# Kernel optimization log

Measured on AMD Instinct MI355X. Metric: run time of the kernel, lower is better.

The kernel has to match this reference:

```python
import jax, jax.numpy as jnp
import numpy as np

B, S, H = 4, 2048, 1024
NH, HD = 16, 64
FF = 4096
EPS = 1e-5

def _ln(x, g, b):
    m = jnp.mean(x, axis=-1, keepdims=True)
    v = jnp.var(x, axis=-1, keepdims=True)
    return (x - m) * jax.lax.rsqrt(v + EPS) * g + b

def setup_inputs() -> dict:
    key = jax.random.key(0)
    ks = jax.random.split(key, 12)
    sc = 0.02
    return {
        "hidden_states": jax.random.normal(ks[0], (B, S, H), jnp.float32),
        "Wq": jax.random.normal(ks[1], (H, H), jnp.float32) * sc,
        "bq": jnp.zeros((H,), jnp.float32),
        "Wk": jax.random.normal(ks[2], (H, H), jnp.float32) * sc,
        "bk": jnp.zeros((H,), jnp.float32),
        "Wv": jax.random.normal(ks[3], (H, H), jnp.float32) * sc,
        "bv": jnp.zeros((H,), jnp.float32),
        "Wi": jax.random.normal(ks[4], (H, FF), jnp.float32) * sc,
        "bi": jnp.zeros((FF,), jnp.float32),
        "Wo": jax.random.normal(ks[5], (FF, H), jnp.float32) * sc,
        "bo": jnp.zeros((H,), jnp.float32),
        "g1": jnp.ones((H,), jnp.float32),
        "b1": jnp.zeros((H,), jnp.float32),
        "g2": jnp.ones((H,), jnp.float32),
        "b2": jnp.zeros((H,), jnp.float32),
    }

def reference(hidden_states, Wq, bq, Wk, bk, Wv, bv, Wi, bi, Wo, bo, g1, b1, g2, b2):
    x = hidden_states
    # projections -> [B, NH, S, HD]
    def split(t):
        return t.reshape(B, S, NH, HD).transpose(0, 2, 1, 3)
    q = split(x @ Wq + bq)
    k = split(x @ Wk + bk)
    v = split(x @ Wv + bv)
    scores = jnp.einsum('bhqd,bhkd->bhqk', q, k) / jnp.sqrt(jnp.float32(HD))
    probs = jax.nn.softmax(scores, axis=-1)
    ctx = jnp.einsum('bhqk,bhkd->bhqd', probs, v)
    attn_out = ctx.transpose(0, 2, 1, 3).reshape(B, S, H)
    h = _ln(x + attn_out, g1, b1)
    ffn = jax.nn.gelu(h @ Wi + bi, approximate=False) @ Wo + bo
    return _ln(h + ffn, g2, b2)
```

## Files before the change

### kernel.cpp

```cpp
#include <hip/hip_runtime.h>

#define B_  4
#define S_  2048
#define H_  1024
#define NH_ 16
#define HD_ 64
#define FF_ 4096
#define M_  (B_*S_)

typedef __bf16 bf16x8 __attribute__((ext_vector_type(8)));
typedef float  f32x4  __attribute__((ext_vector_type(4)));
typedef unsigned short ushort8v __attribute__((ext_vector_type(8)));
typedef unsigned short ushort4v __attribute__((ext_vector_type(4)));

typedef __attribute__((address_space(1))) void GVOID;
typedef __attribute__((address_space(3))) void LVOID;

__device__ __forceinline__ void g2l16(const void* g, void* l) {
  __builtin_amdgcn_global_load_lds((GVOID*)g, (LVOID*)l, 16, 0, 0);
}

#define MFMA16(a, b, c) __builtin_amdgcn_mfma_f32_16x16x32_bf16(a, b, c, 0, 0, 0)

#if __has_builtin(__builtin_amdgcn_exp2f)
#define EXP2(x) __builtin_amdgcn_exp2f(x)
#else
#define EXP2(x) exp2f(x)
#endif

__device__ __forceinline__ unsigned short f2bf(float f) {
  unsigned int u = __float_as_uint(f);
  u += 0x7fffu + ((u >> 16) & 1u);
  return (unsigned short)(u >> 16);
}
__device__ __forceinline__ float bf2f(unsigned short h) {
  return __uint_as_float(((unsigned int)h) << 16);
}

__device__ __forceinline__ float gelu_fast(float v) {
  float y = 0.7978845608f * (v + 0.044715f * v * v * v);
  float e = EXP2(y * 2.8853900818f);
  float th = 1.0f - 2.0f / (e + 1.0f);
  return 0.5f * v * (1.0f + th);
}

__device__ __forceinline__ void xcd_swz(int& bx, int& by) {
  int gx = gridDim.x;
  int flat = by * gx + bx;
  int cpx = (gx * gridDim.y) >> 3;
  int swz = (flat & 7) * cpx + (flat >> 3);
  bx = swz % gx;
  by = swz / gx;
}

__device__ __forceinline__ void xcd_swzT(int& bx, int& by) {
  int gy = gridDim.y;
  int flat = bx * gy + by;
  int cpx = (gridDim.x * gy) >> 3;
  int swz = (flat & 7) * cpx + (flat >> 3);
  by = swz % gy;
  bx = swz / gy;
}

__global__ __launch_bounds__(256) void cast_f32_bf16(const float* __restrict__ in,
                                                     unsigned short* __restrict__ out,
                                                     int n4) {
  int i = blockIdx.x * 256 + threadIdx.x;
  if (i >= n4) return;
  float4 v = reinterpret_cast<const float4*>(in)[i];
  ushort4v o;
  o[0] = f2bf(v.x); o[1] = f2bf(v.y); o[2] = f2bf(v.z); o[3] = f2bf(v.w);
  reinterpret_cast<ushort4v*>(out)[i] = o;
}

__global__ __launch_bounds__(256) void prep_weights(const float* __restrict__ Wq,
                                                    const float* __restrict__ Wk,
                                                    const float* __restrict__ Wv,
                                                    const float* __restrict__ Wi,
                                                    const float* __restrict__ Wo,
                                                    unsigned short* __restrict__ WqkvT,
                                                    unsigned short* __restrict__ WiT,
                                                    unsigned short* __restrict__ WoT) {
  __shared__ float t[32][33];
  int id = blockIdx.x;
  const float* in; unsigned short* out; int R, C, bx, by;
  if (id < 3072) {
    int seg = id >> 10, rem = id & 1023;
    in = (seg == 0) ? Wq : (seg == 1) ? Wk : Wv;
    out = WqkvT + (size_t)seg * H_ * H_;
    R = H_; C = H_;
    bx = rem & 31; by = rem >> 5;
  } else if (id < 3072 + 4096) {
    int rem = id - 3072;
    in = Wi; out = WiT; R = H_; C = FF_;
    bx = rem & 127; by = rem >> 7;
  } else {
    int rem = id - 3072 - 4096;
    in = Wo; out = WoT; R = FF_; C = H_;
    bx = rem & 31; by = rem >> 5;
  }
  bx *= 32; by *= 32;
  const int tx = threadIdx.x & 31, ty = threadIdx.x >> 5;
#pragma unroll
  for (int i = 0; i < 32; i += 8)
    t[ty + i][tx] = in[(size_t)(by + ty + i) * C + bx + tx];
  __syncthreads();
#pragma unroll
  for (int i = 0; i < 32; i += 8)
    out[(size_t)(bx + ty + i) * R + by + tx] = f2bf(t[tx][ty + i]);
}

#define ALOAD(bufv, mf, ks)                                                      \
  *reinterpret_cast<const bf16x8*>((char*)As + (bufv)*32768 + wm*16384 +         \
      ((mf)*16 + lr)*128 + (((((ks)*4 + kg)) ^ (lr & 7)) * 16))
#define BLOAD(bufv, nf, ks)                                                      \
  *reinterpret_cast<const bf16x8*>((char*)Bs + (bufv)*32768 + bh*16384 +         \
      (brow0 + (nf)*16 + lr)*128 + (((((ks)*4 + kg)) ^ (lr & 7)) * 16))

#define PH_MFMA(MF0)                                                             \
  __builtin_amdgcn_s_barrier();                                                  \
  asm volatile("s_waitcnt lgkmcnt(0)" ::: "memory");                             \
  __builtin_amdgcn_s_setprio(1);                                                 \
  _Pragma("unroll")                                                              \
  for (int nf = 0; nf < 4; ++nf) {                                               \
    acc[MF0][nf]     = MFMA16(a_[0][0], bfr[nf][0], acc[MF0][nf]);               \
    acc[MF0][nf]     = MFMA16(a_[0][1], bfr[nf][1], acc[MF0][nf]);               \
    acc[MF0 + 1][nf] = MFMA16(a_[1][0], bfr[nf][0], acc[MF0 + 1][nf]);           \
    acc[MF0 + 1][nf] = MFMA16(a_[1][1], bfr[nf][1], acc[MF0 + 1][nf]);           \
  }                                                                              \
  __builtin_amdgcn_s_setprio(0);

#define GEMM256_CORE(A_, Bt_, LDK_, NKT_, KOFF_)                                 \
  __shared__ unsigned short As[2][2][128 * 64];                                  \
  __shared__ unsigned short Bs[2][2][128 * 64];                                  \
  const int tid  = threadIdx.x;                                                  \
  const int wave = tid >> 6;                                                     \
  const int lane = tid & 63;                                                     \
  const int kg   = lane >> 4;                                                    \
  const int lr   = lane & 15;                                                    \
  const int wm   = wave >> 2;                                                    \
  const int wn   = wave & 3;                                                     \
  const int bh   = wn >> 1;                                                      \
  const int brow0 = (wn & 1) * 64;                                               \
  const int sr = lane >> 3;                                                      \
  const int sc = ((lane & 7) ^ sr) * 8;                                          \
  const unsigned short* sA = &A_[(size_t)(m0 + wave * 8 + sr) * LDK_ + KOFF_ + sc];  \
  const unsigned short* sB = &Bt_[(size_t)(n0 + wave * 8 + sr) * LDK_ + KOFF_ + sc]; \
  char* ldsA = (char*)&As[0][0][0] + wave * 1024;                                \
  char* ldsB = (char*)&Bs[0][0][0] + wave * 1024;                                \
  const size_t rkI = (size_t)64 * LDK_;                                          \
  const size_t rhK = (size_t)128 * LDK_;                                         \
  f32x4 acc[8][4] = {};                                                          \
  const int nkt = (NKT_);                                                        \
  g2l16(sA,             ldsA);                                                   \
  g2l16(sA + rkI,       ldsA + 8192);                                            \
  g2l16(sA + rhK,       ldsA + 16384);                                           \
  g2l16(sA + rhK + rkI, ldsA + 16384 + 8192);                                    \
  g2l16(sB,             ldsB);                                                   \
  g2l16(sB + rkI,       ldsB + 8192);                                            \
  g2l16(sB + rhK,       ldsB + 16384);                                           \
  g2l16(sB + rhK + rkI, ldsB + 16384 + 8192);                                    \
  g2l16(sB + 64,             ldsB + 32768);                                      \
  g2l16(sB + rkI + 64,       ldsB + 32768 + 8192);                               \
  g2l16(sB + rhK + 64,       ldsB + 32768 + 16384);                              \
  g2l16(sB + rhK + rkI + 64, ldsB + 32768 + 16384 + 8192);                       \
  asm volatile("s_waitcnt vmcnt(4)" ::: "memory");                               \
  __builtin_amdgcn_s_barrier();                                                  \
  for (int c = 0; c < nkt; ++c) {                                                \
    const int buf = c & 1;                                                       \
    const bool stgA = (c + 1 < nkt);                                             \
    const bool stgB = (c + 2 < nkt);                                             \
    const size_t kA = (size_t)(c + 1) * 64;                                      \
    const size_t kB = (size_t)(c + 2) * 64;                                      \
    bf16x8 bfr[4][2];                                                            \
    bf16x8 a_[2][2];                                                             \
    _Pragma("unroll")                                                            \
    for (int nf = 0; nf < 4; ++nf) {                                             \
      bfr[nf][0] = BLOAD(buf, nf, 0);                                            \
      bfr[nf][1] = BLOAD(buf, nf, 1);                                            \
    }                                                                            \
    a_[0][0] = ALOAD(buf, 0, 0); a_[0][1] = ALOAD(buf, 0, 1);                    \
    a_[1][0] = ALOAD(buf, 1, 0); a_[1][1] = ALOAD(buf, 1, 1);                    \
    if (stgA) {                                                                  \
      g2l16(sA + kA,       ldsA + (buf ^ 1) * 32768);                            \
      g2l16(sA + rkI + kA, ldsA + (buf ^ 1) * 32768 + 8192);                     \
    }                                                                            \
    PH_MFMA(0)                                                                   \
    __builtin_amdgcn_s_barrier();                                                \
    a_[0][0] = ALOAD(buf, 2, 0); a_[0][1] = ALOAD(buf, 2, 1);                    \
    a_[1][0] = ALOAD(buf, 3, 0); a_[1][1] = ALOAD(buf, 3, 1);                    \
    if (stgA) {                                                                  \
      g2l16(sA + rhK + kA,       ldsA + (buf ^ 1) * 32768 + 16384);              \
      g2l16(sA + rhK + rkI + kA, ldsA + (buf ^ 1) * 32768 + 16384 + 8192);       \
    }                                                                            \
    PH_MFMA(2)                                                                   \
    __builtin_amdgcn_s_barrier();                                                \
    a_[0][0] = ALOAD(buf, 4, 0); a_[0][1] = ALOAD(buf, 4, 1);                    \
    a_[1][0] = ALOAD(buf, 5, 0); a_[1][1] = ALOAD(buf, 5, 1);                    \
    if (stgB) {                                                                  \
      g2l16(sB + kB,       ldsB + buf * 32768);                                  \
      g2l16(sB + rkI + kB, ldsB + buf * 32768 + 8192);                           \
    }                                                                            \
    PH_MFMA(4)                                                                   \
    __builtin_amdgcn_s_barrier();                                                \
    a_[0][0] = ALOAD(buf, 6, 0); a_[0][1] = ALOAD(buf, 6, 1);                    \
    a_[1][0] = ALOAD(buf, 7, 0); a_[1][1] = ALOAD(buf, 7, 1);                    \
    if (stgB) {                                                                  \
      g2l16(sB + rhK + kB,       ldsB + buf * 32768 + 16384);                    \
      g2l16(sB + rhK + rkI + kB, ldsB + buf * 32768 + 16384 + 8192);             \
    }                                                                            \
    PH_MFMA(6)                                                                   \
    if (c < nkt - 2)       asm volatile("s_waitcnt vmcnt(4)" ::: "memory");      \
    else if (c == nkt - 2) asm volatile("s_waitcnt vmcnt(0)" ::: "memory");      \
    __builtin_amdgcn_s_barrier();                                                \
  }

template<int ACT, int OUT_F32>
__global__ __launch_bounds__(512, 1) void gemm256_tn(const unsigned short* __restrict__ A,
                                                     const unsigned short* __restrict__ Bt,
                                                     const float* __restrict__ bias,
                                                     void* __restrict__ C,
                                                     int M, int N, int K) {
  int bx = blockIdx.x, by = blockIdx.y;
  xcd_swzT(bx, by);
  const int z = blockIdx.z;
  const int Klen = K / gridDim.z;
  const int Koff = z * Klen;
  const float* biasEff = (z == 0) ? bias : nullptr;
  const int m0 = bx * 256;
  const int n0 = by * 256;
  GEMM256_CORE(A, Bt, K, Klen >> 6, Koff)

  float* Cf = (float*)C + (size_t)z * M * N;
#pragma unroll
  for (int mf = 0; mf < 8; ++mf) {
#pragma unroll
    for (int nf = 0; nf < 4; ++nf) {
      int col = n0 + wn * 64 + nf * 16 + lr;
      float bc = biasEff ? biasEff[col] : 0.0f;
#pragma unroll
      for (int r = 0; r < 4; ++r) {
        int row = m0 + wm * 128 + mf * 16 + kg * 4 + r;
        float v = acc[mf][nf][r] + bc;
        if (ACT == 1) v = gelu_fast(v);
        if (OUT_F32) Cf[(size_t)row * N + col] = v;
        else reinterpret_cast<unsigned short*>(C)[(size_t)row * N + col] = f2bf(v);
      }
    }
  }
}

__global__ __launch_bounds__(512, 1) void gemm256_qkv(const unsigned short* __restrict__ A,
                                                      const unsigned short* __restrict__ Bt,
                                                      const float* __restrict__ bq,
                                                      const float* __restrict__ bk,
                                                      const float* __restrict__ bv,
                                                      unsigned short* __restrict__ qb,
                                                      unsigned short* __restrict__ kb,
                                                      unsigned short* __restrict__ vt,
                                                      float qscale) {
  int bx = blockIdx.x, by = blockIdx.y;
  xcd_swzT(bx, by);
  const int m0 = bx * 256;
  const int n0 = by * 256;
  GEMM256_CORE(A, Bt, H_, H_ >> 6, 0)

#pragma unroll
  for (int mf = 0; mf < 8; ++mf) {
#pragma unroll
    for (int nf = 0; nf < 4; ++nf) {
      int colb = n0 + wn * 64 + nf * 16;
      int col  = colb + lr;
      int seg  = colb >> 10;
      int row0 = m0 + wm * 128 + mf * 16 + kg * 4;
      if (seg == 0) {
        float bc = bq[col];
#pragma unroll
        for (int r = 0; r < 4; ++r)
          qb[(size_t)(row0 + r) * H_ + col] = f2bf((acc[mf][nf][r] + bc) * qscale);
      } else if (seg == 1) {
        float bc = bk[col - 1024];
#pragma unroll
        for (int r = 0; r < 4; ++r)
          kb[(size_t)(row0 + r) * H_ + col - 1024] = f2bf(acc[mf][nf][r] + bc);
      } else {
        float bc = bv[col - 2048];
        ushort4v o;
#pragma unroll
        for (int r = 0; r < 4; ++r) o[r] = f2bf(acc[mf][nf][r] + bc);
        *reinterpret_cast<ushort4v*>(&vt[(size_t)(col - 2048) * M_ + row0]) = o;
      }
    }
  }
}

__global__ __launch_bounds__(512) void attn_fwd(const unsigned short* __restrict__ Q,
                                                const unsigned short* __restrict__ Kb,
                                                const unsigned short* __restrict__ VT,
                                                unsigned short* __restrict__ O) {
  __shared__ unsigned short Ks[2][64 * 64];
  __shared__ unsigned short Vs[2][64 * 64];
  __shared__ __bf16 Ps[8][32 * 64];

  const int tid  = threadIdx.x;
  const int wave = tid >> 6;
  const int lane = tid & 63;
  const int kg   = lane >> 4;
  const int lr   = lane & 15;
  int bx = blockIdx.x, by = blockIdx.y;
  xcd_swz(bx, by);
  const int b  = by >> 4;
  const int h  = by & 15;
  const size_t rowbase = (size_t)b * S_;
  const int hcol = h * 64;
  const int bcol0 = b * S_;
  const int q0 = bx * 256 + wave * 32;

  const int rT = wave * 8 + (lane >> 3);
  const int ce = ((lane & 7) * 8) ^ (((lane >> 3) & 7) << 3);
  const int fswz = (lr & 7) << 3;

  bf16x8 qf[2][2];
#pragma unroll
  for (int sub = 0; sub < 2; ++sub)
#pragma unroll
    for (int d = 0; d < 2; ++d)
      qf[sub][d] = *reinterpret_cast<const bf16x8*>(
          &Q[(rowbase + q0 + sub * 16 + lr) * H_ + hcol + d * 32 + kg * 8]);

  bf16x8 ones;
#pragma unroll
  for (int i = 0; i < 8; ++i) ones[i] = (__bf16)1.0f;

  const f32x4 cinit = {-8.0f, -8.0f, -8.0f, -8.0f};

  f32x4 ctx[2][4] = {};
  f32x4 lsum[2] = {};

  auto stage = [&](int kt, int buf) {
    g2l16(&Kb[(rowbase + kt * 64 + rT) * H_ + hcol + ce], &Ks[buf][wave * 512]);
    g2l16(&VT[(size_t)(hcol + rT) * M_ + bcol0 + kt * 64 + ce], &Vs[buf][wave * 512]);
  };

  stage(0, 0);
  __syncthreads();

  const int NT = S_ / 64;
  for (int kt = 0; kt < NT; ++kt) {
    const int cur = kt & 1;
    if (kt + 1 < NT) stage(kt + 1, cur ^ 1);

    f32x4 s0[4], s1[4];
    __builtin_amdgcn_s_setprio(1);
#pragma unroll
    for (int nf = 0; nf < 4; ++nf) {
      int row = nf * 16 + lr;
      bf16x8 kf0 = *reinterpret_cast<const bf16x8*>(&Ks[cur][row * 64 + ((kg * 8) ^ fswz)]);
      bf16x8 kf1 = *reinterpret_cast<const bf16x8*>(&Ks[cur][row * 64 + ((32 + kg * 8) ^ fswz)]);
      f32x4 z0 = cinit, z1 = cinit;
      z0 = MFMA16(qf[0][0], kf0, z0);
      z0 = MFMA16(qf[0][1], kf1, z0);
      z1 = MFMA16(qf[1][0], kf0, z1);
      z1 = MFMA16(qf[1][1], kf1, z1);
      s0[nf] = z0;
      s1[nf] = z1;
    }
    __builtin_amdgcn_s_setprio(0);

#pragma unroll
    for (int nf = 0; nf < 4; ++nf)
#pragma unroll
      for (int r = 0; r < 4; ++r) {
        int row = kg * 4 + r;
        Ps[wave][row * 64 + ((nf * 16 + lr) ^ ((row & 7) << 3))] =
            (__bf16)EXP2(s0[nf][r]);
        Ps[wave][(16 + row) * 64 + ((nf * 16 + lr) ^ ((row & 7) << 3))] =
            (__bf16)EXP2(s1[nf][r]);
      }
    bf16x8 p00 = *reinterpret_cast<const bf16x8*>(
        &Ps[wave][lr * 64 + ((kg ^ (lr & 7)) << 3)]);
    bf16x8 p01 = *reinterpret_cast<const bf16x8*>(
        &Ps[wave][lr * 64 + (((4 + kg) ^ (lr & 7)) << 3)]);
    bf16x8 p10 = *reinterpret_cast<const bf16x8*>(
        &Ps[wave][(16 + lr) * 64 + ((kg ^ (lr & 7)) << 3)]);
    bf16x8 p11 = *reinterpret_cast<const bf16x8*>(
        &Ps[wave][(16 + lr) * 64 + (((4 + kg) ^ (lr & 7)) << 3)]);

    __builtin_amdgcn_s_setprio(1);
#pragma unroll
    for (int df = 0; df < 4; ++df) {
      int row = df * 16 + lr;
      bf16x8 vf0 = *reinterpret_cast<const bf16x8*>(&Vs[cur][row * 64 + ((kg * 8) ^ fswz)]);
      bf16x8 vf1 = *reinterpret_cast<const bf16x8*>(&Vs[cur][row * 64 + ((32 + kg * 8) ^ fswz)]);
      ctx[0][df] = MFMA16(p00, vf0, ctx[0][df]);
      ctx[0][df] = MFMA16(p01, vf1, ctx[0][df]);
      ctx[1][df] = MFMA16(p10, vf0, ctx[1][df]);
      ctx[1][df] = MFMA16(p11, vf1, ctx[1][df]);
    }
    lsum[0] = MFMA16(p00, ones, lsum[0]);
    lsum[0] = MFMA16(p01, ones, lsum[0]);
    lsum[1] = MFMA16(p10, ones, lsum[1]);
    lsum[1] = MFMA16(p11, ones, lsum[1]);
    __builtin_amdgcn_s_setprio(0);

    __syncthreads();
  }

#pragma unroll
  for (int sub = 0; sub < 2; ++sub)
#pragma unroll
    for (int r = 0; r < 4; ++r) {
      float rl = 1.0f / lsum[sub][r];
#pragma unroll
      for (int df = 0; df < 4; ++df) {
        float v = ctx[sub][df][r] * rl;
        O[(rowbase + q0 + sub * 16 + kg * 4 + r) * H_ + hcol + df * 16 + lr] = f2bf(v);
      }
    }
}

__global__ __launch_bounds__(256) void add_ln_b(const float* __restrict__ X,
                                                const unsigned short* __restrict__ Y,
                                                const float* __restrict__ g,
                                                const float* __restrict__ beta,
                                                unsigned short* __restrict__ outB) {
  const int row = blockIdx.x;
  const int tid = threadIdx.x;
  const int wave = tid >> 6, lane = tid & 63;
  __shared__ float red[8];

  const size_t base = (size_t)row * H_ + tid * 4;
  float4 xv = *reinterpret_cast<const float4*>(&X[base]);
  ushort4v yv = *reinterpret_cast<const ushort4v*>(&Y[base]);
  float vals[4] = {xv.x + bf2f(yv[0]), xv.y + bf2f(yv[1]),
                   xv.z + bf2f(yv[2]), xv.w + bf2f(yv[3])};
  float s = 0.0f, s2 = 0.0f;
#pragma unroll
  for (int i = 0; i < 4; ++i) { s += vals[i]; s2 += vals[i] * vals[i]; }
#pragma unroll
  for (int off = 32; off; off >>= 1) { s += __shfl_xor(s, off); s2 += __shfl_xor(s2, off); }
  if (lane == 0) { red[wave * 2] = s; red[wave * 2 + 1] = s2; }
  __syncthreads();
  s  = red[0] + red[2] + red[4] + red[6];
  s2 = red[1] + red[3] + red[5] + red[7];
  float mean = s * (1.0f / H_);
  float var  = s2 * (1.0f / H_) - mean * mean;
  float rstd = rsqrtf(var + 1e-5f);

  float4 gv = *reinterpret_cast<const float4*>(&g[tid * 4]);
  float4 bv = *reinterpret_cast<const float4*>(&beta[tid * 4]);
  float gs[4] = {gv.x, gv.y, gv.z, gv.w};
  float bs[4] = {bv.x, bv.y, bv.z, bv.w};
  ushort4v ob;
#pragma unroll
  for (int i = 0; i < 4; ++i)
    ob[i] = f2bf((vals[i] - mean) * rstd * gs[i] + bs[i]);
  *reinterpret_cast<ushort4v*>(&outB[base]) = ob;
}

__global__ __launch_bounds__(256) void add_ln3(const unsigned short* __restrict__ X,
                                               const float* __restrict__ Y0,
                                               const float* __restrict__ Y1,
                                               const float* __restrict__ g,
                                               const float* __restrict__ beta,
                                               float* __restrict__ outF) {
  const int row = blockIdx.x;
  const int tid = threadIdx.x;
  const int wave = tid >> 6, lane = tid & 63;
  __shared__ float red[8];

  const size_t base = (size_t)row * H_ + tid * 4;
  ushort4v xv = *reinterpret_cast<const ushort4v*>(&X[base]);
  float4 y0 = *reinterpret_cast<const float4*>(&Y0[base]);
  float4 y1 = *reinterpret_cast<const float4*>(&Y1[base]);
  float vals[4] = {bf2f(xv[0]) + y0.x + y1.x, bf2f(xv[1]) + y0.y + y1.y,
                   bf2f(xv[2]) + y0.z + y1.z, bf2f(xv[3]) + y0.w + y1.w};
  float s = 0.0f, s2 = 0.0f;
#pragma unroll
  for (int i = 0; i < 4; ++i) { s += vals[i]; s2 += vals[i] * vals[i]; }
#pragma unroll
  for (int off = 32; off; off >>= 1) { s += __shfl_xor(s, off); s2 += __shfl_xor(s2, off); }
  if (lane == 0) { red[wave * 2] = s; red[wave * 2 + 1] = s2; }
  __syncthreads();
  s  = red[0] + red[2] + red[4] + red[6];
  s2 = red[1] + red[3] + red[5] + red[7];
  float mean = s * (1.0f / H_);
  float var  = s2 * (1.0f / H_) - mean * mean;
  float rstd = rsqrtf(var + 1e-5f);

  float4 gv = *reinterpret_cast<const float4*>(&g[tid * 4]);
  float4 bv = *reinterpret_cast<const float4*>(&beta[tid * 4]);
  float4 of;
  of.x = (vals[0] - mean) * rstd * gv.x + bv.x;
  of.y = (vals[1] - mean) * rstd * gv.y + bv.y;
  of.z = (vals[2] - mean) * rstd * gv.z + bv.z;
  of.w = (vals[3] - mean) * rstd * gv.w + bv.w;
  *reinterpret_cast<float4*>(&outF[base]) = of;
}

extern "C" void kernel_launch(void* const* d_in, const int* in_sizes, int n_in,
                              void* d_out, int out_size, void* d_ws, size_t ws_size,
                              hipStream_t stream) {
  const float* x  = (const float*)d_in[0];
  const float* Wq = (const float*)d_in[1];
  const float* bq = (const float*)d_in[2];
  const float* Wk = (const float*)d_in[3];
  const float* bk = (const float*)d_in[4];
  const float* Wv = (const float*)d_in[5];
  const float* bv = (const float*)d_in[6];
  const float* Wi = (const float*)d_in[7];
  const float* bi = (const float*)d_in[8];
  const float* Wo = (const float*)d_in[9];
  const float* bo = (const float*)d_in[10];
  const float* g1 = (const float*)d_in[11];
  const float* b1 = (const float*)d_in[12];
  const float* g2 = (const float*)d_in[13];
  const float* b2 = (const float*)d_in[14];

  unsigned char* ws = (unsigned char*)d_ws;
  size_t off = 0;
  auto alloc = [&](size_t bytes) { size_t o = off; off += (bytes + 255) & ~(size_t)255; return o; };

  unsigned short* WqkvT = (unsigned short*)(ws + alloc((size_t)3 * H_ * H_ * 2));
  unsigned short* WiT   = (unsigned short*)(ws + alloc((size_t)H_ * FF_ * 2));
  unsigned short* WoT   = (unsigned short*)(ws + alloc((size_t)FF_ * H_ * 2));
  unsigned short* hb    = (unsigned short*)(ws + alloc((size_t)M_ * H_ * 2));
  unsigned short* f1    = (unsigned short*)(ws + alloc((size_t)M_ * FF_ * 2));
  unsigned short* xb    = (unsigned short*)(ws + alloc((size_t)M_ * H_ * 2));
  unsigned short* qb    = (unsigned short*)(ws + alloc((size_t)M_ * H_ * 2));
  unsigned short* kb    = (unsigned short*)(ws + alloc((size_t)M_ * H_ * 2));
  unsigned short* vt    = (unsigned short*)(ws + alloc((size_t)M_ * H_ * 2));
  unsigned short* ao    = (unsigned short*)(ws + alloc((size_t)M_ * H_ * 2));
  float*          f2p   = (float*)xb;

  {
    int n4 = (int)((size_t)M_ * H_ / 4);
    cast_f32_bf16<<<(n4 + 255) / 256, 256, 0, stream>>>(x, xb, n4);
  }
  prep_weights<<<3072 + 4096 + 4096, 256, 0, stream>>>(Wq, Wk, Wv, Wi, Wo,
                                                       WqkvT, WiT, WoT);

  const float QSCALE = 0.125f * 1.44269504088896340736f;

  gemm256_qkv<<<dim3(M_ / 256, 3072 / 256), 512, 0, stream>>>(xb, WqkvT, bq, bk, bv,
                                                              qb, kb, vt, QSCALE);

  attn_fwd<<<dim3(S_ / 256, B_ * NH_), 512, 0, stream>>>(qb, kb, vt, ao);

  add_ln_b<<<M_, 256, 0, stream>>>(x, ao, g1, b1, hb);

  gemm256_tn<1, 0><<<dim3(M_ / 256, FF_ / 256), 512, 0, stream>>>(hb, WiT, bi, f1, M_, FF_, H_);
  gemm256_tn<0, 1><<<dim3(M_ / 256, H_ / 256, 2), 512, 0, stream>>>(f1, WoT, bo, f2p, M_, H_, FF_);

  add_ln3<<<M_, 256, 0, stream>>>(hb, f2p, f2p + (size_t)M_ * H_, g2, b2, (float*)d_out);
}
```

Measured before the change: 425.3 us.

## Unroll GEMM K-loop by two, store split-K partials in bf16, unroll attention loop

The GEMM core's K loop is manually unrolled by two with constant buffer indices, and the last two tiles are peeled so the per-iteration wait-count branches go away. The split-K FFN output partials are now written in bf16 instead of fp32, which halves partial-sum traffic into the final add+LayerNorm; that kernel now reads bf16 partials. The attention KV loop also gets an unroll-2 pragma. Rounding the partials to bf16 loses precision, and the peeled loop assumes an even tile count of at least two.

```diff
diff --git a/kernel.cpp b/kernel.cpp
--- a/kernel.cpp
+++ b/kernel.cpp
@@ -117,6 +117,10 @@
   *reinterpret_cast<const bf16x8*>((char*)Bs + (bufv)*32768 + bh*16384 +         \
       (brow0 + (nf)*16 + lr)*128 + (((((ks)*4 + kg)) ^ (lr & 7)) * 16))
 
+#define W4 asm volatile("s_waitcnt vmcnt(4)" ::: "memory")
+#define W0 asm volatile("s_waitcnt vmcnt(0)" ::: "memory")
+#define WN ((void)0)
+
 #define PH_MFMA(MF0)                                                             \
   __builtin_amdgcn_s_barrier();                                                  \
   asm volatile("s_waitcnt lgkmcnt(0)" ::: "memory");                             \
@@ -129,6 +133,51 @@
     acc[MF0 + 1][nf] = MFMA16(a_[1][1], bfr[nf][1], acc[MF0 + 1][nf]);           \
   }                                                                              \
   __builtin_amdgcn_s_setprio(0);
+
+#define GEMM_TILE(bufL, STGA, STGB, WAITOP)                                      \
+  {                                                                              \
+    bf16x8 bfr[4][2];                                                            \
+    bf16x8 a_[2][2];                                                             \
+    _Pragma("unroll")                                                            \
+    for (int nf = 0; nf < 4; ++nf) {                                             \
+      bfr[nf][0] = BLOAD(bufL, nf, 0);                                           \
+      bfr[nf][1] = BLOAD(bufL, nf, 1);                                           \
+    }                                                                            \
+    a_[0][0] = ALOAD(bufL, 0, 0); a_[0][1] = ALOAD(bufL, 0, 1);                  \
+    a_[1][0] = ALOAD(bufL, 1, 0); a_[1][1] = ALOAD(bufL, 1, 1);                  \
+    if (STGA) {                                                                  \
+      g2l16(sA + kA,       ldsA + ((bufL) ^ 1) * 32768);                         \
+      g2l16(sA + rkI + kA, ldsA + ((bufL) ^ 1) * 32768 + 8192);                  \
+    }                                                                            \
+    PH_MFMA(0)                                                                   \
+    __builtin_amdgcn_s_barrier();                                                \
+    a_[0][0] = ALOAD(bufL, 2, 0); a_[0][1] = ALOAD(bufL, 2, 1);                  \
+    a_[1][0] = ALOAD(bufL, 3, 0); a_[1][1] = ALOAD(bufL, 3, 1);                  \
+    if (STGA) {                                                                  \
+      g2l16(sA + rhK + kA,       ldsA + ((bufL) ^ 1) * 32768 + 16384);           \
+      g2l16(sA + rhK + rkI + kA, ldsA + ((bufL) ^ 1) * 32768 + 16384 + 8192);    \
+    }                                                                            \
+    PH_MFMA(2)                                                                   \
+    __builtin_amdgcn_s_barrier();                                                \
+    a_[0][0] = ALOAD(bufL, 4, 0); a_[0][1] = ALOAD(bufL, 4, 1);                  \
+    a_[1][0] = ALOAD(bufL, 5, 0); a_[1][1] = ALOAD(bufL, 5, 1);                  \
+    if (STGB) {                                                                  \
+      g2l16(sB + kB,       ldsB + (bufL) * 32768);                               \
+      g2l16(sB + rkI + kB, ldsB + (bufL) * 32768 + 8192);                        \
+    }                                                                            \
+    PH_MFMA(4)                                                                   \
+    __builtin_amdgcn_s_barrier();                                                \
+    a_[0][0] = ALOAD(bufL, 6, 0); a_[0][1] = ALOAD(bufL, 6, 1);                  \
+    a_[1][0] = ALOAD(bufL, 7, 0); a_[1][1] = ALOAD(bufL, 7, 1);                  \
+    if (STGB) {                                                                  \
+      g2l16(sB + rhK + kB,       ldsB + (bufL) * 32768 + 16384);                 \
+      g2l16(sB + rhK + rkI + kB, ldsB + (bufL) * 32768 + 16384 + 8192);          \
+    }                                                                            \
+    PH_MFMA(6)                                                                   \
+    WAITOP;                                                                      \
+    __builtin_amdgcn_s_barrier();                                                \
+    kA += 64; kB += 64;                                                          \
+  }
 
 #define GEMM256_CORE(A_, Bt_, LDK_, NKT_, KOFF_)                                 \
   __shared__ unsigned short As[2][2][128 * 64];                                  \
@@ -152,6 +201,7 @@
   const size_t rhK = (size_t)128 * LDK_;                                         \
   f32x4 acc[8][4] = {};                                                          \
   const int nkt = (NKT_);                                                        \
+  size_t kA = 64, kB = 128;                                                      \
   g2l16(sA,             ldsA);                                                   \
   g2l16(sA + rkI,       ldsA + 8192);                                            \
   g2l16(sA + rhK,       ldsA + 16384);                                           \
@@ -164,74 +214,32 @@
   g2l16(sB + rkI + 64,       ldsB + 32768 + 8192);                               \
   g2l16(sB + rhK + 64,       ldsB + 32768 + 16384);                              \
   g2l16(sB + rhK + rkI + 64, ldsB + 32768 + 16384 + 8192);                       \
-  asm volatile("s_waitcnt vmcnt(4)" ::: "memory");                               \
+  W4;                                                                            \
   __builtin_amdgcn_s_barrier();                                                  \
-  for (int c = 0; c < nkt; ++c) {                                                \
-    const int buf = c & 1;                                                       \
-    const bool stgA = (c + 1 < nkt);                                             \
-    const bool stgB = (c + 2 < nkt);                                             \
-    const size_t kA = (size_t)(c + 1) * 64;                                      \
-    const size_t kB = (size_t)(c + 2) * 64;                                      \
-    bf16x8 bfr[4][2];                                                            \
-    bf16x8 a_[2][2];                                                             \
-    _Pragma("unroll")                                                            \
-    for (int nf = 0; nf < 4; ++nf) {                                             \
-      bfr[nf][0] = BLOAD(buf, nf, 0);                                            \
-      bfr[nf][1] = BLOAD(buf, nf, 1);                                            \
-    }                                                                            \
-    a_[0][0] = ALOAD(buf, 0, 0); a_[0][1] = ALOAD(buf, 0, 1);                    \
-    a_[1][0] = ALOAD(buf, 1, 0); a_[1][1] = ALOAD(buf, 1, 1);                    \
-    if (stgA) {                                                                  \
-      g2l16(sA + kA,       ldsA + (buf ^ 1) * 32768);                            \
-      g2l16(sA + rkI + kA, ldsA + (buf ^ 1) * 32768 + 8192);                     \
-    }                                                                            \
-    PH_MFMA(0)                                                                   \
-    __builtin_amdgcn_s_barrier();                                                \
-    a_[0][0] = ALOAD(buf, 2, 0); a_[0][1] = ALOAD(buf, 2, 1);                    \
-    a_[1][0] = ALOAD(buf, 3, 0); a_[1][1] = ALOAD(buf, 3, 1);                    \
-    if (stgA) {                                                                  \
-      g2l16(sA + rhK + kA,       ldsA + (buf ^ 1) * 32768 + 16384);              \
-      g2l16(sA + rhK + rkI + kA, ldsA + (buf ^ 1) * 32768 + 16384 + 8192);       \
-    }                                                                            \
-    PH_MFMA(2)                                                                   \
-    __builtin_amdgcn_s_barrier();                                                \
-    a_[0][0] = ALOAD(buf, 4, 0); a_[0][1] = ALOAD(buf, 4, 1);                    \
-    a_[1][0] = ALOAD(buf, 5, 0); a_[1][1] = ALOAD(buf, 5, 1);                    \
-    if (stgB) {                                                                  \
-      g2l16(sB + kB,       ldsB + buf * 32768);                                  \
-      g2l16(sB + rkI + kB, ldsB + buf * 32768 + 8192);                           \
-    }                                                                            \
-    PH_MFMA(4)                                                                   \
-    __builtin_amdgcn_s_barrier();                                                \
-    a_[0][0] = ALOAD(buf, 6, 0); a_[0][1] = ALOAD(buf, 6, 1);                    \
-    a_[1][0] = ALOAD(buf, 7, 0); a_[1][1] = ALOAD(buf, 7, 1);                    \
-    if (stgB) {                                                                  \
-      g2l16(sB + rhK + kB,       ldsB + buf * 32768 + 16384);                    \
-      g2l16(sB + rhK + rkI + kB, ldsB + buf * 32768 + 16384 + 8192);             \
-    }                                                                            \
-    PH_MFMA(6)                                                                   \
-    if (c < nkt - 2)       asm volatile("s_waitcnt vmcnt(4)" ::: "memory");      \
-    else if (c == nkt - 2) asm volatile("s_waitcnt vmcnt(0)" ::: "memory");      \
-    __builtin_amdgcn_s_barrier();                                                \
-  }
-
-template<int ACT, int OUT_F32>
+  for (int c = 0; c < nkt - 2; c += 2) {        \
+    GEMM_TILE(0, 1, 1, W4)                                                       \
+    GEMM_TILE(1, 1, 1, W4)                                                       \
+  }                                                                              \
+  GEMM_TILE(0, 1, 0, W0)             \
+  GEMM_TILE(1, 0, 0, WN)
+
+template<int ACT, int SPLITK>
 __global__ __launch_bounds__(512, 1) void gemm256_tn(const unsigned short* __restrict__ A,
                                                      const unsigned short* __restrict__ Bt,
                                                      const float* __restrict__ bias,
-                                                     void* __restrict__ C,
+                                                     unsigned short* __restrict__ C,
                                                      int M, int N, int K) {
   int bx = blockIdx.x, by = blockIdx.y;
   xcd_swzT(bx, by);
-  const int z = blockIdx.z;
-  const int Klen = K / gridDim.z;
+  const int z = SPLITK ? blockIdx.z : 0;
+  const int Klen = SPLITK ? (K / gridDim.z) : K;
   const int Koff = z * Klen;
   const float* biasEff = (z == 0) ? bias : nullptr;
   const int m0 = bx * 256;
   const int n0 = by * 256;
   GEMM256_CORE(A, Bt, K, Klen >> 6, Koff)
 
-  float* Cf = (float*)C + (size_t)z * M * N;
+  unsigned short* Cz = C + (size_t)z * M * N;
 #pragma unroll
   for (int mf = 0; mf < 8; ++mf) {
 #pragma unroll
@@ -243,8 +251,7 @@
         int row = m0 + wm * 128 + mf * 16 + kg * 4 + r;
         float v = acc[mf][nf][r] + bc;
         if (ACT == 1) v = gelu_fast(v);
-        if (OUT_F32) Cf[(size_t)row * N + col] = v;
-        else reinterpret_cast<unsigned short*>(C)[(size_t)row * N + col] = f2bf(v);
+        Cz[(size_t)row * N + col] = f2bf(v);
       }
     }
   }
@@ -346,6 +353,7 @@
   __syncthreads();
 
   const int NT = S_ / 64;
+#pragma unroll 2
   for (int kt = 0; kt < NT; ++kt) {
     const int cur = kt & 1;
     if (kt + 1 < NT) stage(kt + 1, cur ^ 1);
@@ -459,8 +467,8 @@
 }
 
 __global__ __launch_bounds__(256) void add_ln3(const unsigned short* __restrict__ X,
-                                               const float* __restrict__ Y0,
-                                               const float* __restrict__ Y1,
+                                               const unsigned short* __restrict__ Y0,
+                                               const unsigned short* __restrict__ Y1,
                                                const float* __restrict__ g,
                                                const float* __restrict__ beta,
                                                float* __restrict__ outF) {
@@ -471,10 +479,12 @@
 
   const size_t base = (size_t)row * H_ + tid * 4;
   ushort4v xv = *reinterpret_cast<const ushort4v*>(&X[base]);
-  float4 y0 = *reinterpret_cast<const float4*>(&Y0[base]);
-  float4 y1 = *reinterpret_cast<const float4*>(&Y1[base]);
-  float vals[4] = {bf2f(xv[0]) + y0.x + y1.x, bf2f(xv[1]) + y0.y + y1.y,
-                   bf2f(xv[2]) + y0.z + y1.z, bf2f(xv[3]) + y0.w + y1.w};
+  ushort4v y0 = *reinterpret_cast<const ushort4v*>(&Y0[base]);
+  ushort4v y1 = *reinterpret_cast<const ushort4v*>(&Y1[base]);
+  float vals[4];
+#pragma unroll
+  for (int i = 0; i < 4; ++i)
+    vals[i] = bf2f(xv[i]) + bf2f(y0[i]) + bf2f(y1[i]);
   float s = 0.0f, s2 = 0.0f;
 #pragma unroll
   for (int i = 0; i < 4; ++i) { s += vals[i]; s2 += vals[i] * vals[i]; }
@@ -531,7 +541,7 @@
   unsigned short* kb    = (unsigned short*)(ws + alloc((size_t)M_ * H_ * 2));
   unsigned short* vt    = (unsigned short*)(ws + alloc((size_t)M_ * H_ * 2));
   unsigned short* ao    = (unsigned short*)(ws + alloc((size_t)M_ * H_ * 2));
-  float*          f2p   = (float*)xb;
+  unsigned short* f2p   = xb;
 
   {
     int n4 = (int)((size_t)M_ * H_ / 4);
```

Result: faster. 394.9 us, median of 2 (-7.1%).
